# Kernel optimization log

Hardware: AMD Instinct MI355X
Metric: run time of the kernel (lower is better)

Reference implementation:

```python
import jax, jax.numpy as jnp
import numpy as np
import math

EPS = 1e-5

def _ln(x, g, b):
    m = jnp.mean(x, axis=-1, keepdims=True)
    v = jnp.var(x, axis=-1, keepdims=True)
    return (x - m) * jax.lax.rsqrt(v + EPS) * g + b

def _rn_layer(x, W, g, b, A, Bb, Rw):
    # x: (B,S,in) -> (B,S,out). W: (out,in), A: (out,basis), Bb: (basis,out)
    S = x.shape[1]
    basis_dim = Bb.shape[0]
    n = _ln(x @ W.T, g, b)                      # (B,S,out)
    j = jnp.arange(S) % basis_dim               # (S,)
    Bv = Bb[j]                                  # (S,out)
    scal = jnp.einsum('bsd,sd->bs', n, Bv)      # (B,S)
    Av = A[:, j].T                              # (S,out)
    nf = scal[..., None] * Av                   # (B,S,out)
    res = x if Rw is None else x @ Rw.T
    return nf + res

def _ts_layer(x, M, g, b, P, Rw):
    # x: (B,S,in) -> (B,S,out). M: (out,in), P: (out,out,G)
    S = x.shape[1]
    D, _, G = P.shape
    t = _ln(x @ M.T, g, b)                      # (B,S,out)
    k = jnp.arange(S, dtype=jnp.float32)
    periods = (jnp.arange(D, dtype=jnp.float32)[:, None, None] * (D * G)
               + jnp.arange(D, dtype=jnp.float32)[None, :, None] * G
               + jnp.arange(G, dtype=jnp.float32)[None, None, :] + 2.0)  # (D,D,G)
    phi = jnp.cos(2.0 * math.pi * k[:, None, None, None] / periods)       # (S,D,D,G)
    # Nk[b,s,i] = sum_{j,g} P[i,j,g] * t[b,s,j] * phi[s,i,j,g]
    Wp = jnp.einsum('ijg,sijg->sij', P, phi)    # (S,D,D)
    Nk = jnp.einsum('sij,bsj->bsi', Wp, t)      # (B,S,D)
    return Nk + x @ Rw.T

def setup_inputs() -> dict:
    key = jax.random.key(0)
    ks = jax.random.split(key, 16)
    B, S = 2, 2048
    d0, d1, d2 = 512, 64, 512        # input_dim, ts out, final out
    bas1, G, bas3 = 64, 8, 64
    u = lambda k, sh, a: jax.random.uniform(k, sh, jnp.float32, -a, a)
    inp = {
        'x':  jax.random.normal(ks[0], (B, S, d0), jnp.float32),
        # Layer 1: RN 512->512 (in==out -> no residual proj)
        'W1': u(ks[1], (d0, d0), 0.1),
        'g1': jnp.ones((d0,), jnp.float32),
        'b1': jnp.zeros((d0,), jnp.float32),
        'A1': u(ks[2], (d0, bas1), 0.1),
        'B1': u(ks[3], (bas1, d0), 0.1),
        # Layer 2: TS 512->64
        'M2': u(ks[4], (d1, d0), 0.5),
        'g2': jnp.ones((d1,), jnp.float32),
        'b2': jnp.zeros((d1,), jnp.float32),
        'P2': u(ks[5], (d1, d1, G), 0.1),
        'R2': u(ks[6], (d1, d0), 0.1),
        # Layer 3: RN 64->512
        'W3': u(ks[7], (d2, d1), 0.1),
        'g3': jnp.ones((d2,), jnp.float32),
        'b3': jnp.zeros((d2,), jnp.float32),
        'A3': u(ks[8], (d2, bas3), 0.1),
        'B3': u(ks[9], (bas3, d2), 0.1),
        'R3': u(ks[10], (d2, d1), 0.1),
    }
    return inp

def reference(x, W1, g1, b1, A1, B1, M2, g2, b2, P2, R2, W3, g3, b3, A3, B3, R3):
    h = _rn_layer(x, W1, g1, b1, A1, B1, None)   # (B,S,512), identity residual
    h = _ts_layer(h, M2, g2, b2, P2, R2)         # (B,S,64)
    h = _rn_layer(h, W3, g3, b3, A3, B3, R3)     # (B,S,512)
    return h
```

## Files before the change

### kernel.cpp

```cpp
#include <hip/hip_runtime.h>
#include <math.h>

#define SEQ  2048
#define ROWS 4096
#define D0   512
#define D1   64

typedef short bf8 __attribute__((ext_vector_type(8)));
typedef float f4  __attribute__((ext_vector_type(4)));

__device__ __forceinline__ unsigned short f2bf(float f) {
    unsigned u = __float_as_uint(f);
    return (unsigned short)((u + 0x7fffu + ((u >> 16) & 1u)) >> 16);
}
__device__ __forceinline__ float bf2f(unsigned short u) {
    return __uint_as_float((unsigned)u << 16);
}
__device__ __forceinline__ void hilo(float f, unsigned short& h, unsigned short& l) {
    h = f2bf(f);
    float fh = bf2f(h);
    l = f2bf(f - fh);
}
__device__ __forceinline__ void cv4h(unsigned short* dh, int idx, float4 v) {
    ushort4 hv;
    hv.x = f2bf(v.x); hv.y = f2bf(v.y); hv.z = f2bf(v.z); hv.w = f2bf(v.w);
    *(ushort4*)(dh + idx) = hv;
}

__device__ __forceinline__ void async16(const void* g, void* l) {
    __builtin_amdgcn_global_load_lds(
        (const __attribute__((address_space(1))) unsigned int*)g,
        (__attribute__((address_space(3))) unsigned int*)l, 16, 0, 0);
}

__global__ __launch_bounds__(256) void convk(
        const float* __restrict__ x,  const float* __restrict__ W1,
        const float* __restrict__ M2, const float* __restrict__ R2,
        const float* __restrict__ W3, const float* __restrict__ R3,
        const float* __restrict__ A1, const float* __restrict__ A3,
        unsigned short* __restrict__ xh,
        unsigned short* __restrict__ W1h,
        unsigned short* __restrict__ C2h,
        unsigned short* __restrict__ C3h,
        float* __restrict__ A1T, float* __restrict__ A3T) {
    int c = blockIdx.x, tid = threadIdx.x;
    if (c < 1216) {
        const float* src; unsigned short* dh; int off;
        if      (c < 1024) { src = x;  dh = xh;          off = c; }
        else if (c < 1152) { src = W1; dh = W1h;         off = c - 1024; }
        else if (c < 1168) { src = M2; dh = C2h;         off = c - 1152; }
        else if (c < 1184) { src = R2; dh = C2h + 32768; off = c - 1168; }
        else if (c < 1200) { src = W3; dh = C3h;         off = c - 1184; }
        else               { src = R3; dh = C3h + 32768; off = c - 1200; }
        int base = off * 2048 + tid * 4;
        cv4h(dh, base,        *(const float4*)(src + base));
        cv4h(dh, base + 1024, *(const float4*)(src + base + 1024));
    } else {
        int gid = (c - 1216) * 256 + tid;
        int i = gid >> 6, j = gid & 63;
        A1T[j * 512 + i] = A1[gid];
        A3T[j * 512 + i] = A3[gid];
    }
}

template<bool ALO, int OM>
__global__ __launch_bounds__(256, 4) void gemm128t(
        const unsigned short* __restrict__ Ah, const unsigned short* __restrict__ Al,
        const unsigned short* __restrict__ Wh,
        float* __restrict__ Cf, unsigned short* __restrict__ Cb,
        int M, int N, int K, int Ks) {
    __shared__ __align__(16) unsigned short aH[8192];
    __shared__ __align__(16) unsigned short aL[ALO ? 8192 : 16];
    __shared__ __align__(16) unsigned short wH[4096];
    const int tid = threadIdx.x;
    const int wv  = tid >> 6;
    const int ln  = tid & 63;
    const int lm  = ln & 15;
    const int lq  = ln >> 4;
    const int bm  = blockIdx.y * 128;
    const int bn  = blockIdx.x * 64;
    const int k0  = blockIdx.z * Ks;

    f4 acc[2][4] = {};

    for (int kt = 0; kt < Ks; kt += 64) {
        const int kg = k0 + kt;
        __syncthreads();
#pragma unroll
        for (int i = 0; i < 4; ++i) {
            int slot = i * 256 + wv * 64 + ln;
            int row  = slot >> 3;
            int ch   = (slot & 7) ^ (row & 7);
            size_t go = (size_t)(bm + row) * K + kg + ch * 8;
            async16(Ah + go, aH + slot * 8);
            if constexpr (ALO) async16(Al + go, aL + slot * 8);
        }
#pragma unroll
        for (int i = 0; i < 2; ++i) {
            int slot = i * 256 + wv * 64 + ln;
            int row  = slot >> 3;
            int ch   = (slot & 7) ^ (row & 7);
            size_t go = (size_t)(bn + row) * K + kg + ch * 8;
            async16(Wh + go, wH + slot * 8);
        }
        __syncthreads();

#pragma unroll
        for (int kk = 0; kk < 2; ++kk) {
            const int ck = kk * 4 + lq;
            bf8 a_h[2], a_l[2], b_h[4];
#pragma unroll
            for (int t = 0; t < 2; ++t) {
                int r = wv * 32 + t * 16 + lm;
                a_h[t] = *(const bf8*)(aH + r * 64 + ((ck ^ (r & 7)) * 8));
                if constexpr (ALO)
                    a_l[t] = *(const bf8*)(aL + r * 64 + ((ck ^ (r & 7)) * 8));
            }
#pragma unroll
            for (int u = 0; u < 4; ++u) {
                int rb = u * 16 + lm;
                b_h[u] = *(const bf8*)(wH + rb * 64 + ((ck ^ (rb & 7)) * 8));
            }
#pragma unroll
            for (int t = 0; t < 2; ++t)
#pragma unroll
                for (int u = 0; u < 4; ++u) {
                    acc[t][u] = __builtin_amdgcn_mfma_f32_16x16x32_bf16(a_h[t], b_h[u], acc[t][u], 0, 0, 0);
                    if constexpr (ALO)
                        acc[t][u] = __builtin_amdgcn_mfma_f32_16x16x32_bf16(a_l[t], b_h[u], acc[t][u], 0, 0, 0);
                }
        }
    }

#pragma unroll
    for (int t = 0; t < 2; ++t)
#pragma unroll
        for (int u = 0; u < 4; ++u) {
            int row = bm + wv * 32 + t * 16 + lq * 4;
            int col = bn + u * 16 + lm;
#pragma unroll
            for (int r = 0; r < 4; ++r) {
                float v = acc[t][u][r];
                if constexpr (OM == 0) {
                    Cf[(size_t)blockIdx.z * M * N + (size_t)(row + r) * N + col] = v;
                } else if constexpr (OM == 1) {
                    Cb[(size_t)blockIdx.z * M * N + (size_t)(row + r) * N + col] = f2bf(v);
                } else {
                    if (col < 512) Cb[(size_t)(row + r) * 512 + col] = f2bf(v);
                    else           Cf[(size_t)(row + r) * 512 + col - 512] = v;
                }
            }
        }
}

__global__ __launch_bounds__(256) void lnrn(
        const unsigned short* __restrict__ Yb0,
        const unsigned short* __restrict__ Yb1,
        const float* __restrict__ RES,
        const float* __restrict__ g, const float* __restrict__ be,
        const float* __restrict__ Bb, const float* __restrict__ AaT,
        float* __restrict__ outf,
        unsigned short* __restrict__ outh, unsigned short* __restrict__ outl) {
    const int row = blockIdx.x * 4 + (threadIdx.x >> 6);
    const int l = threadIdx.x & 63;
    const int c = l * 8;
    ushort4 ua = *(const ushort4*)(Yb0 + (size_t)row * D0 + c);
    ushort4 ub = *(const ushort4*)(Yb0 + (size_t)row * D0 + c + 4);
    float4 y0, y1;
    y0.x = bf2f(ua.x); y0.y = bf2f(ua.y); y0.z = bf2f(ua.z); y0.w = bf2f(ua.w);
    y1.x = bf2f(ub.x); y1.y = bf2f(ub.y); y1.z = bf2f(ub.z); y1.w = bf2f(ub.w);
    if (Yb1) {
        ushort4 va = *(const ushort4*)(Yb1 + (size_t)row * D0 + c);
        ushort4 vb = *(const ushort4*)(Yb1 + (size_t)row * D0 + c + 4);
        y0.x += bf2f(va.x); y0.y += bf2f(va.y); y0.z += bf2f(va.z); y0.w += bf2f(va.w);
        y1.x += bf2f(vb.x); y1.y += bf2f(vb.y); y1.z += bf2f(vb.z); y1.w += bf2f(vb.w);
    }
    float sum = y0.x + y0.y + y0.z + y0.w + y1.x + y1.y + y1.z + y1.w;
    float ssq = y0.x*y0.x + y0.y*y0.y + y0.z*y0.z + y0.w*y0.w
              + y1.x*y1.x + y1.y*y1.y + y1.z*y1.z + y1.w*y1.w;
#pragma unroll
    for (int m = 1; m < 64; m <<= 1) {
        sum += __shfl_xor(sum, m, 64);
        ssq += __shfl_xor(ssq, m, 64);
    }
    float mean = sum * (1.0f / 512.0f);
    float var  = ssq * (1.0f / 512.0f) - mean * mean;
    float rstd = rsqrtf(var + 1e-5f);
    float4 g0 = *(const float4*)(g + c),  g1v = *(const float4*)(g + c + 4);
    float4 e0 = *(const float4*)(be + c), e1  = *(const float4*)(be + c + 4);
    float4 n0, n1;
    n0.x = (y0.x - mean) * rstd * g0.x  + e0.x;
    n0.y = (y0.y - mean) * rstd * g0.y  + e0.y;
    n0.z = (y0.z - mean) * rstd * g0.z  + e0.z;
    n0.w = (y0.w - mean) * rstd * g0.w  + e0.w;
    n1.x = (y1.x - mean) * rstd * g1v.x + e1.x;
    n1.y = (y1.y - mean) * rstd * g1v.y + e1.y;
    n1.z = (y1.z - mean) * rstd * g1v.z + e1.z;
    n1.w = (y1.w - mean) * rstd * g1v.w + e1.w;
    const int jm = row & 63;
    const float* bb = Bb + jm * D0 + c;
    float4 b0 = *(const float4*)bb, b1v = *(const float4*)(bb + 4);
    float p = n0.x*b0.x + n0.y*b0.y + n0.z*b0.z + n0.w*b0.w
            + n1.x*b1v.x + n1.y*b1v.y + n1.z*b1v.z + n1.w*b1v.w;
#pragma unroll
    for (int m = 1; m < 64; m <<= 1) p += __shfl_xor(p, m, 64);
    const float* av = AaT + jm * D0 + c;
    float4 a0 = *(const float4*)av, a1 = *(const float4*)(av + 4);
    const float* rs = RES + (size_t)row * D0 + c;
    float4 r0 = *(const float4*)rs, r1 = *(const float4*)(rs + 4);
    float4 v0, v1;
    v0.x = p*a0.x + r0.x; v0.y = p*a0.y + r0.y; v0.z = p*a0.z + r0.z; v0.w = p*a0.w + r0.w;
    v1.x = p*a1.x + r1.x; v1.y = p*a1.y + r1.y; v1.z = p*a1.z + r1.z; v1.w = p*a1.w + r1.w;
    if (outf) {
        *(float4*)(outf + (size_t)row * D0 + c)     = v0;
        *(float4*)(outf + (size_t)row * D0 + c + 4) = v1;
    } else {
        ushort4 h0, l0, h1, l1;
        hilo(v0.x, h0.x, l0.x); hilo(v0.y, h0.y, l0.y);
        hilo(v0.z, h0.z, l0.z); hilo(v0.w, h0.w, l0.w);
        hilo(v1.x, h1.x, l1.x); hilo(v1.y, h1.y, l1.y);
        hilo(v1.z, h1.z, l1.z); hilo(v1.w, h1.w, l1.w);
        *(ushort4*)(outh + (size_t)row * D0 + c)     = h0;
        *(ushort4*)(outl + (size_t)row * D0 + c)     = l0;
        *(ushort4*)(outh + (size_t)row * D0 + c + 4) = h1;
        *(ushort4*)(outl + (size_t)row * D0 + c + 4) = l1;
    }
}

#define C2S 524288
__global__ __launch_bounds__(256) void lnt(
        const float* __restrict__ C2, const float* __restrict__ g2,
        const float* __restrict__ b2,
        float* __restrict__ t, float* __restrict__ rsum) {
    const int r = blockIdx.x * 4 + (threadIdx.x >> 6);
    const int j = threadIdx.x & 63;
    size_t base = (size_t)r * 128 + j;
    float v = 0.f, rv = 0.f;
#pragma unroll
    for (int z = 0; z < 4; ++z) {
        v  += C2[(size_t)z * C2S + base];
        rv += C2[(size_t)z * C2S + base + 64];
    }
    float sum = v, ssq = v * v;
#pragma unroll
    for (int m = 1; m < 64; m <<= 1) {
        sum += __shfl_xor(sum, m, 64);
        ssq += __shfl_xor(ssq, m, 64);
    }
    float mean = sum * (1.0f / 64.0f);
    float var  = ssq * (1.0f / 64.0f) - mean * mean;
    float rstd = rsqrtf(var + 1e-5f);
    t[r * 64 + j]    = (v - mean) * rstd * g2[j] + b2[j];
    rsum[r * 64 + j] = rv;
}

__global__ __launch_bounds__(256) void tsk2(
        const float* __restrict__ t, const float* __restrict__ rsum,
        const float* __restrict__ P,
        unsigned short* __restrict__ Hh, unsigned short* __restrict__ Hl) {
    const int bid = blockIdx.x;
    const int i   = bid >> 3;
    const int sg  = bid & 7;
    const int w   = threadIdx.x >> 6;
    const int ln  = threadIdx.x & 63;
    const int s0  = sg * 256 + w * 64;
    const int idx = i * 64 + ln;
    const float* pp = P + idx * 8;
    const float sf0 = (float)s0;

    float k2c[8], ca[8], cb[8];
#pragma unroll
    for (int g = 0; g < 8; ++g) {
        float pf   = (float)(idx * 8 + g + 2);
        float invp = __builtin_amdgcn_rcpf(pf);
        k2c[g] = 2.0f * __builtin_amdgcn_cosf(invp);
        float q0 = floorf(sf0 * invp);
        float r0 = fmaf(-q0, pf, sf0);
        float f0 = r0 * invp; f0 -= floorf(f0);
        float c0 = __builtin_amdgcn_cosf(f0);
        float sf1 = sf0 + 1.0f;
        float q1 = floorf(sf1 * invp);
        float r1 = fmaf(-q1, pf, sf1);
        float f1 = r1 * invp; f1 -= floorf(f1);
        float c1 = __builtin_amdgcn_cosf(f1);
        float Pv = pp[g];
        ca[g] = Pv * c0;
        cb[g] = Pv * c1;
    }

    const int tb = s0 * 64 + ln;
    float t0c = t[tb], t1c = t[131072 + tb];
    float res0 = 0.f, res1 = 0.f;

    for (int st = 0; st < 64; st += 2) {
        float t0n  = t[tb + (st + 1) * 64];
        float t1n  = t[131072 + tb + (st + 1) * 64];
        float ws = ((ca[0] + ca[1]) + (ca[2] + ca[3]))
                 + ((ca[4] + ca[5]) + (ca[6] + ca[7]));
#pragma unroll
        for (int g = 0; g < 8; ++g) ca[g] = fmaf(k2c[g], cb[g], -ca[g]);
        float v0 = ws * t0c, v1 = ws * t1c;
#pragma unroll
        for (int m = 1; m < 64; m <<= 1) {
            v0 += __shfl_xor(v0, m, 64);
            v1 += __shfl_xor(v1, m, 64);
        }
        res0 = (ln == st) ? v0 : res0;
        res1 = (ln == st) ? v1 : res1;
        float t0n2 = t[tb + (st + 2) * 64];
        float t1n2 = t[131072 + tb + (st + 2) * 64];
        float ws2 = ((cb[0] + cb[1]) + (cb[2] + cb[3]))
                  + ((cb[4] + cb[5]) + (cb[6] + cb[7]));
#pragma unroll
        for (int g = 0; g < 8; ++g) cb[g] = fmaf(k2c[g], ca[g], -cb[g]);
        float v0b = ws2 * t0n, v1b = ws2 * t1n;
#pragma unroll
        for (int m = 1; m < 64; m <<= 1) {
            v0b += __shfl_xor(v0b, m, 64);
            v1b += __shfl_xor(v1b, m, 64);
        }
        res0 = (ln == st + 1) ? v0b : res0;
        res1 = (ln == st + 1) ? v1b : res1;
        t0c = t0n2; t1c = t1n2;
    }

    const int s = s0 + ln;
    {
        float v = res0 + rsum[(size_t)s * 64 + i];
        unsigned short h, l; hilo(v, h, l);
        Hh[(size_t)s * 64 + i] = h; Hl[(size_t)s * 64 + i] = l;
        float v1e = res1 + rsum[(size_t)(SEQ + s) * 64 + i];
        hilo(v1e, h, l);
        Hh[(size_t)(SEQ + s) * 64 + i] = h; Hl[(size_t)(SEQ + s) * 64 + i] = l;
    }
}

extern "C" void kernel_launch(void* const* d_in, const int* in_sizes, int n_in,
                              void* d_out, int out_size, void* d_ws, size_t ws_size,
                              hipStream_t stream) {
    const float* x  = (const float*)d_in[0];
    const float* W1 = (const float*)d_in[1];
    const float* g1 = (const float*)d_in[2];
    const float* b1 = (const float*)d_in[3];
    const float* A1 = (const float*)d_in[4];
    const float* B1 = (const float*)d_in[5];
    const float* M2 = (const float*)d_in[6];
    const float* g2 = (const float*)d_in[7];
    const float* b2 = (const float*)d_in[8];
    const float* P2 = (const float*)d_in[9];
    const float* R2 = (const float*)d_in[10];
    const float* W3 = (const float*)d_in[11];
    const float* g3 = (const float*)d_in[12];
    const float* b3 = (const float*)d_in[13];
    const float* A3 = (const float*)d_in[14];
    const float* B3 = (const float*)d_in[15];
    const float* R3 = (const float*)d_in[16];

    float* ws = (float*)d_ws;
    float* C2   = ws;
    float* C3r  = ws + 2097152;
    float* t    = ws + 4194304;
    float* rsum = ws + 4456448;
    float* A1T  = ws + 4718592;
    float* A3T  = ws + 4751360;
    unsigned short* us = (unsigned short*)(ws + 4784128);
    unsigned short* xh   = us;
    unsigned short* h1h  = us + 2097152;
    unsigned short* h1l  = us + 4194304;
    unsigned short* W1h  = us + 6291456;
    unsigned short* Wc2h = us + 6553600;
    unsigned short* Wc3h = us + 6619136;
    unsigned short* h2h  = us + 6684672;
    unsigned short* h2l  = us + 6946816;
    unsigned short* C1b  = us + 7208960;
    unsigned short* C3n  = us + 11403264;

    dim3 blk(256);

    convk<<<1344, blk, 0, stream>>>(x, W1, M2, R2, W3, R3, A1, A3,
                                    xh, W1h, Wc2h, Wc3h, A1T, A3T);

    gemm128t<false, 1><<<dim3(8, 32, 2), blk, 0, stream>>>(
        xh, xh, W1h, nullptr, C1b, ROWS, 512, 512, 256);
    lnrn<<<1024, blk, 0, stream>>>(C1b, C1b + (size_t)ROWS * 512, x,
                                   g1, b1, B1, A1T, nullptr, h1h, h1l);

    gemm128t<true, 0><<<dim3(2, 32, 4), blk, 0, stream>>>(
        h1h, h1l, Wc2h, C2, nullptr, ROWS, 128, 512, 128);
    lnt<<<1024, blk, 0, stream>>>(C2, g2, b2, t, rsum);
    tsk2<<<512, blk, 0, stream>>>(t, rsum, P2, h2h, h2l);

    gemm128t<true, 2><<<dim3(16, 32, 1), blk, 0, stream>>>(
        h2h, h2l, Wc3h, C3r, C3n, ROWS, 1024, 64, 64);
    lnrn<<<1024, blk, 0, stream>>>(C3n, nullptr, C3r, g3, b3, B3, A3T,
                                   (float*)d_out, nullptr, nullptr);
}
```

Measured before the change: 152.1 us.

## Fuse all stages into one cooperative persistent megakernel with grid syncs

Replaces the eight separate kernel launches with a single cooperative kernel of 256 blocks of 512 threads, in which each block acts as two virtual 256-thread workers and the stages are separated by grid.sync(). The goal is to remove per-launch overhead and inter-kernel gaps. The cost is that the GEMM tiles are remapped onto a fixed 256-block grid, which changes occupancy: each block uses a larger LDS footprint and 512 threads. Some stages leave blocks idle, for example the second GEMM uses only 128 blocks. If the cooperative launch fails, the code falls back to the old multi-kernel path.

```diff
diff --git a/kernel.cpp b/kernel.cpp
--- a/kernel.cpp
+++ b/kernel.cpp
@@ -1,10 +1,14 @@
 #include <hip/hip_runtime.h>
+#include <hip/hip_cooperative_groups.h>
 #include <math.h>
+
+namespace cg = cooperative_groups;
 
 #define SEQ  2048
 #define ROWS 4096
 #define D0   512
 #define D1   64
+#define C2S  524288
 
 typedef short bf8 __attribute__((ext_vector_type(8)));
 typedef float f4  __attribute__((ext_vector_type(4)));
@@ -31,6 +35,383 @@
     __builtin_amdgcn_global_load_lds(
         (const __attribute__((address_space(1))) unsigned int*)g,
         (__attribute__((address_space(3))) unsigned int*)l, 16, 0, 0);
+}
+
+struct KArgs {
+    const float *x, *W1, *g1, *b1, *A1, *B1;
+    const float *M2, *g2, *b2, *P2, *R2;
+    const float *W3, *g3, *b3, *A3, *B3, *R3;
+    float* out;
+    float* ws;
+};
+
+__device__ __forceinline__ void conv_v(int c, int tid, const KArgs& a,
+        unsigned short* xh, unsigned short* W1h,
+        unsigned short* C2h, unsigned short* C3h,
+        float* A1T, float* A3T) {
+    if (c < 1216) {
+        const float* src; unsigned short* dh; int off;
+        if      (c < 1024) { src = a.x;  dh = xh;          off = c; }
+        else if (c < 1152) { src = a.W1; dh = W1h;         off = c - 1024; }
+        else if (c < 1168) { src = a.M2; dh = C2h;         off = c - 1152; }
+        else if (c < 1184) { src = a.R2; dh = C2h + 32768; off = c - 1168; }
+        else if (c < 1200) { src = a.W3; dh = C3h;         off = c - 1184; }
+        else               { src = a.R3; dh = C3h + 32768; off = c - 1200; }
+        int base = off * 2048 + tid * 4;
+        cv4h(dh, base,        *(const float4*)(src + base));
+        cv4h(dh, base + 1024, *(const float4*)(src + base + 1024));
+    } else {
+        int gid = (c - 1216) * 256 + tid;
+        int i = gid >> 6, j = gid & 63;
+        A1T[j * 512 + i] = a.A1[gid];
+        A3T[j * 512 + i] = a.A3[gid];
+    }
+}
+
+template<bool ALO, int OM>
+__device__ __forceinline__ void gemm512(
+        const unsigned short* __restrict__ Ah, const unsigned short* __restrict__ Al,
+        const unsigned short* __restrict__ Wh,
+        float* __restrict__ Cf, unsigned short* __restrict__ Cb,
+        int N, int K, int Ks, int bm, int bn, int k0,
+        unsigned short* aH, unsigned short* aL, unsigned short* wHh) {
+    const int t   = threadIdx.x;
+    const int tid = t & 255;
+    const int ln  = t & 63;
+    const int wv  = (t >> 6) & 3;
+    const int lm  = ln & 15;
+    const int lq  = ln >> 4;
+
+    f4 acc[2][4] = {};
+
+    for (int kt = 0; kt < Ks; kt += 64) {
+        const int kg = k0 + kt;
+        __syncthreads();
+#pragma unroll
+        for (int i = 0; i < 2; ++i) {
+            int slot = i * 512 + t;
+            int row  = slot >> 3;
+            int ch   = (slot & 7) ^ (row & 7);
+            size_t go = (size_t)(bm + row) * K + kg + ch * 8;
+            async16(Ah + go, aH + slot * 8);
+            if constexpr (ALO) async16(Al + go, aL + slot * 8);
+        }
+#pragma unroll
+        for (int i = 0; i < 2; ++i) {
+            int slot = i * 256 + tid;
+            int row  = slot >> 3;
+            int ch   = (slot & 7) ^ (row & 7);
+            size_t go = (size_t)(bn + row) * K + kg + ch * 8;
+            async16(Wh + go, wHh + slot * 8);
+        }
+        __syncthreads();
+
+#pragma unroll
+        for (int kk = 0; kk < 2; ++kk) {
+            const int ck = kk * 4 + lq;
+            bf8 a_h[2], a_l[2], b_h[4];
+#pragma unroll
+            for (int t2 = 0; t2 < 2; ++t2) {
+                int r = wv * 32 + t2 * 16 + lm;
+                a_h[t2] = *(const bf8*)(aH + r * 64 + ((ck ^ (r & 7)) * 8));
+                if constexpr (ALO)
+                    a_l[t2] = *(const bf8*)(aL + r * 64 + ((ck ^ (r & 7)) * 8));
+            }
+#pragma unroll
+            for (int u = 0; u < 4; ++u) {
+                int rb = u * 16 + lm;
+                b_h[u] = *(const bf8*)(wHh + rb * 64 + ((ck ^ (rb & 7)) * 8));
+            }
+#pragma unroll
+            for (int t2 = 0; t2 < 2; ++t2)
+#pragma unroll
+                for (int u = 0; u < 4; ++u) {
+                    acc[t2][u] = __builtin_amdgcn_mfma_f32_16x16x32_bf16(a_h[t2], b_h[u], acc[t2][u], 0, 0, 0);
+                    if constexpr (ALO)
+                        acc[t2][u] = __builtin_amdgcn_mfma_f32_16x16x32_bf16(a_l[t2], b_h[u], acc[t2][u], 0, 0, 0);
+                }
+        }
+    }
+
+#pragma unroll
+    for (int t2 = 0; t2 < 2; ++t2)
+#pragma unroll
+        for (int u = 0; u < 4; ++u) {
+            int row = bm + wv * 32 + t2 * 16 + lq * 4;
+            int col = bn + u * 16 + lm;
+#pragma unroll
+            for (int r = 0; r < 4; ++r) {
+                float v = acc[t2][u][r];
+                if constexpr (OM == 0) {
+                    Cf[(size_t)(row + r) * N + col] = v;
+                } else if constexpr (OM == 1) {
+                    Cb[(size_t)(row + r) * N + col] = f2bf(v);
+                } else {
+                    if (col < 512) Cb[(size_t)(row + r) * 512 + col] = f2bf(v);
+                    else           Cf[(size_t)(row + r) * 512 + col - 512] = v;
+                }
+            }
+        }
+}
+
+__device__ __forceinline__ void lnrn_v(int vb,
+        const unsigned short* __restrict__ Yb0,
+        const unsigned short* __restrict__ Yb1,
+        const float* __restrict__ RES,
+        const float* __restrict__ g, const float* __restrict__ be,
+        const float* __restrict__ Bb, const float* __restrict__ AaT,
+        float* __restrict__ outf,
+        unsigned short* __restrict__ outh, unsigned short* __restrict__ outl) {
+    const int row = vb * 4 + ((threadIdx.x >> 6) & 3);
+    const int l = threadIdx.x & 63;
+    const int c = l * 8;
+    ushort4 ua = *(const ushort4*)(Yb0 + (size_t)row * D0 + c);
+    ushort4 ub = *(const ushort4*)(Yb0 + (size_t)row * D0 + c + 4);
+    float4 y0, y1;
+    y0.x = bf2f(ua.x); y0.y = bf2f(ua.y); y0.z = bf2f(ua.z); y0.w = bf2f(ua.w);
+    y1.x = bf2f(ub.x); y1.y = bf2f(ub.y); y1.z = bf2f(ub.z); y1.w = bf2f(ub.w);
+    if (Yb1) {
+        ushort4 va = *(const ushort4*)(Yb1 + (size_t)row * D0 + c);
+        ushort4 vb2 = *(const ushort4*)(Yb1 + (size_t)row * D0 + c + 4);
+        y0.x += bf2f(va.x); y0.y += bf2f(va.y); y0.z += bf2f(va.z); y0.w += bf2f(va.w);
+        y1.x += bf2f(vb2.x); y1.y += bf2f(vb2.y); y1.z += bf2f(vb2.z); y1.w += bf2f(vb2.w);
+    }
+    float sum = y0.x + y0.y + y0.z + y0.w + y1.x + y1.y + y1.z + y1.w;
+    float ssq = y0.x*y0.x + y0.y*y0.y + y0.z*y0.z + y0.w*y0.w
+              + y1.x*y1.x + y1.y*y1.y + y1.z*y1.z + y1.w*y1.w;
+#pragma unroll
+    for (int m = 1; m < 64; m <<= 1) {
+        sum += __shfl_xor(sum, m, 64);
+        ssq += __shfl_xor(ssq, m, 64);
+    }
+    float mean = sum * (1.0f / 512.0f);
+    float var  = ssq * (1.0f / 512.0f) - mean * mean;
+    float rstd = rsqrtf(var + 1e-5f);
+    float4 g0 = *(const float4*)(g + c),  g1v = *(const float4*)(g + c + 4);
+    float4 e0 = *(const float4*)(be + c), e1  = *(const float4*)(be + c + 4);
+    float4 n0, n1;
+    n0.x = (y0.x - mean) * rstd * g0.x  + e0.x;
+    n0.y = (y0.y - mean) * rstd * g0.y  + e0.y;
+    n0.z = (y0.z - mean) * rstd * g0.z  + e0.z;
+    n0.w = (y0.w - mean) * rstd * g0.w  + e0.w;
+    n1.x = (y1.x - mean) * rstd * g1v.x + e1.x;
+    n1.y = (y1.y - mean) * rstd * g1v.y + e1.y;
+    n1.z = (y1.z - mean) * rstd * g1v.z + e1.z;
+    n1.w = (y1.w - mean) * rstd * g1v.w + e1.w;
+    const int jm = row & 63;
+    const float* bb = Bb + jm * D0 + c;
+    float4 b0 = *(const float4*)bb, b1v = *(const float4*)(bb + 4);
+    float p = n0.x*b0.x + n0.y*b0.y + n0.z*b0.z + n0.w*b0.w
+            + n1.x*b1v.x + n1.y*b1v.y + n1.z*b1v.z + n1.w*b1v.w;
+#pragma unroll
+    for (int m = 1; m < 64; m <<= 1) p += __shfl_xor(p, m, 64);
+    const float* av = AaT + jm * D0 + c;
+    float4 a0 = *(const float4*)av, a1 = *(const float4*)(av + 4);
+    const float* rs = RES + (size_t)row * D0 + c;
+    float4 r0 = *(const float4*)rs, r1 = *(const float4*)(rs + 4);
+    float4 v0, v1;
+    v0.x = p*a0.x + r0.x; v0.y = p*a0.y + r0.y; v0.z = p*a0.z + r0.z; v0.w = p*a0.w + r0.w;
+    v1.x = p*a1.x + r1.x; v1.y = p*a1.y + r1.y; v1.z = p*a1.z + r1.z; v1.w = p*a1.w + r1.w;
+    if (outf) {
+        *(float4*)(outf + (size_t)row * D0 + c)     = v0;
+        *(float4*)(outf + (size_t)row * D0 + c + 4) = v1;
+    } else {
+        ushort4 h0, l0, h1, l1;
+        hilo(v0.x, h0.x, l0.x); hilo(v0.y, h0.y, l0.y);
+        hilo(v0.z, h0.z, l0.z); hilo(v0.w, h0.w, l0.w);
+        hilo(v1.x, h1.x, l1.x); hilo(v1.y, h1.y, l1.y);
+        hilo(v1.z, h1.z, l1.z); hilo(v1.w, h1.w, l1.w);
+        *(ushort4*)(outh + (size_t)row * D0 + c)     = h0;
+        *(ushort4*)(outl + (size_t)row * D0 + c)     = l0;
+        *(ushort4*)(outh + (size_t)row * D0 + c + 4) = h1;
+        *(ushort4*)(outl + (size_t)row * D0 + c + 4) = l1;
+    }
+}
+
+__device__ __forceinline__ void lnt_v(int vb,
+        const float* __restrict__ C2, const float* __restrict__ g2,
+        const float* __restrict__ b2,
+        float* __restrict__ tv, float* __restrict__ rsum) {
+    const int r = vb * 4 + ((threadIdx.x >> 6) & 3);
+    const int j = threadIdx.x & 63;
+    size_t base = (size_t)r * 128 + j;
+    float v = 0.f, rv = 0.f;
+#pragma unroll
+    for (int z = 0; z < 4; ++z) {
+        v  += C2[(size_t)z * C2S + base];
+        rv += C2[(size_t)z * C2S + base + 64];
+    }
+    float sum = v, ssq = v * v;
+#pragma unroll
+    for (int m = 1; m < 64; m <<= 1) {
+        sum += __shfl_xor(sum, m, 64);
+        ssq += __shfl_xor(ssq, m, 64);
+    }
+    float mean = sum * (1.0f / 64.0f);
+    float var  = ssq * (1.0f / 64.0f) - mean * mean;
+    float rstd = rsqrtf(var + 1e-5f);
+    tv[r * 64 + j]   = (v - mean) * rstd * g2[j] + b2[j];
+    rsum[r * 64 + j] = rv;
+}
+
+__device__ __forceinline__ void tsk2_v(int vb,
+        const float* __restrict__ tv, const float* __restrict__ rsum,
+        const float* __restrict__ P,
+        unsigned short* __restrict__ Hh, unsigned short* __restrict__ Hl) {
+    const int i   = vb >> 3;
+    const int sg  = vb & 7;
+    const int w   = (threadIdx.x >> 6) & 3;
+    const int ln  = threadIdx.x & 63;
+    const int s0  = sg * 256 + w * 64;
+    const int idx = i * 64 + ln;
+    const float* pp = P + idx * 8;
+    const float sf0 = (float)s0;
+
+    float k2c[8], ca[8], cb[8];
+#pragma unroll
+    for (int g = 0; g < 8; ++g) {
+        float pf   = (float)(idx * 8 + g + 2);
+        float invp = __builtin_amdgcn_rcpf(pf);
+        k2c[g] = 2.0f * __builtin_amdgcn_cosf(invp);
+        float q0 = floorf(sf0 * invp);
+        float r0 = fmaf(-q0, pf, sf0);
+        float f0 = r0 * invp; f0 -= floorf(f0);
+        float c0 = __builtin_amdgcn_cosf(f0);
+        float sf1 = sf0 + 1.0f;
+        float q1 = floorf(sf1 * invp);
+        float r1 = fmaf(-q1, pf, sf1);
+        float f1 = r1 * invp; f1 -= floorf(f1);
+        float c1 = __builtin_amdgcn_cosf(f1);
+        float Pv = pp[g];
+        ca[g] = Pv * c0;
+        cb[g] = Pv * c1;
+    }
+
+    const int tb = s0 * 64 + ln;
+    float t0c = tv[tb], t1c = tv[131072 + tb];
+    float res0 = 0.f, res1 = 0.f;
+
+    for (int st = 0; st < 64; st += 2) {
+        float t0n  = tv[tb + (st + 1) * 64];
+        float t1n  = tv[131072 + tb + (st + 1) * 64];
+        float ws = ((ca[0] + ca[1]) + (ca[2] + ca[3]))
+                 + ((ca[4] + ca[5]) + (ca[6] + ca[7]));
+#pragma unroll
+        for (int g = 0; g < 8; ++g) ca[g] = fmaf(k2c[g], cb[g], -ca[g]);
+        float v0 = ws * t0c, v1 = ws * t1c;
+#pragma unroll
+        for (int m = 1; m < 64; m <<= 1) {
+            v0 += __shfl_xor(v0, m, 64);
+            v1 += __shfl_xor(v1, m, 64);
+        }
+        res0 = (ln == st) ? v0 : res0;
+        res1 = (ln == st) ? v1 : res1;
+        float t0n2 = tv[tb + (st + 2) * 64];
+        float t1n2 = tv[131072 + tb + (st + 2) * 64];
+        float ws2 = ((cb[0] + cb[1]) + (cb[2] + cb[3]))
+                  + ((cb[4] + cb[5]) + (cb[6] + cb[7]));
+#pragma unroll
+        for (int g = 0; g < 8; ++g) cb[g] = fmaf(k2c[g], ca[g], -cb[g]);
+        float v0b = ws2 * t0n, v1b = ws2 * t1n;
+#pragma unroll
+        for (int m = 1; m < 64; m <<= 1) {
+            v0b += __shfl_xor(v0b, m, 64);
+            v1b += __shfl_xor(v1b, m, 64);
+        }
+        res0 = (ln == st + 1) ? v0b : res0;
+        res1 = (ln == st + 1) ? v1b : res1;
+        t0c = t0n2; t1c = t1n2;
+    }
+
+    const int s = s0 + ln;
+    {
+        float v = res0 + rsum[(size_t)s * 64 + i];
+        unsigned short h, l; hilo(v, h, l);
+        Hh[(size_t)s * 64 + i] = h; Hl[(size_t)s * 64 + i] = l;
+        float v1e = res1 + rsum[(size_t)(SEQ + s) * 64 + i];
+        hilo(v1e, h, l);
+        Hh[(size_t)(SEQ + s) * 64 + i] = h; Hl[(size_t)(SEQ + s) * 64 + i] = l;
+    }
+}
+
+__global__ __launch_bounds__(512) void megak(KArgs a) {
+    cg::grid_group grid = cg::this_grid();
+    const int t    = threadIdx.x;
+    const int half = t >> 8;
+    const int tid  = t & 255;
+    const int bid  = blockIdx.x;
+    const int wid  = bid * 2 + half;
+
+    __shared__ __align__(16) unsigned short aH[8192];
+    __shared__ __align__(16) unsigned short aL[8192];
+    __shared__ __align__(16) unsigned short wH[2][4096];
+
+    float* ws   = a.ws;
+    float* C2   = ws;
+    float* C3r  = ws + 2097152;
+    float* tbuf = ws + 4194304;
+    float* rsum = ws + 4456448;
+    float* A1T  = ws + 4718592;
+    float* A3T  = ws + 4751360;
+    unsigned short* us = (unsigned short*)(ws + 4784128);
+    unsigned short* xh   = us;
+    unsigned short* h1h  = us + 2097152;
+    unsigned short* h1l  = us + 4194304;
+    unsigned short* W1h  = us + 6291456;
+    unsigned short* Wc2h = us + 6553600;
+    unsigned short* Wc3h = us + 6619136;
+    unsigned short* h2h  = us + 6684672;
+    unsigned short* h2l  = us + 6946816;
+    unsigned short* C1b  = us + 7208960;
+    unsigned short* C3n  = us + 11403264;
+
+    for (int c = wid; c < 1344; c += 512)
+        conv_v(c, tid, a, xh, W1h, Wc2h, Wc3h, A1T, A3T);
+    grid.sync();
+
+    {
+        int bn = (bid & 3) * 128 + half * 64;
+        int bm = ((bid >> 2) & 31) * 128;
+        int bz = bid >> 7;
+        gemm512<false, 1>(xh, xh, W1h, nullptr,
+                          C1b + (size_t)bz * ROWS * 512,
+                          512, 512, 256, bm, bn, bz * 256, aH, aL, wH[half]);
+    }
+    grid.sync();
+
+    for (int vb = wid; vb < 1024; vb += 512)
+        lnrn_v(vb, C1b, C1b + (size_t)ROWS * 512, a.x, a.g1, a.b1, a.B1, A1T,
+               nullptr, h1h, h1l);
+    grid.sync();
+
+    if (bid < 128) {
+        int bn = half * 64;
+        int bm = (bid & 31) * 128;
+        int bz = bid >> 5;
+        gemm512<true, 0>(h1h, h1l, Wc2h,
+                         C2 + (size_t)bz * C2S, nullptr,
+                         128, 512, 128, bm, bn, bz * 128, aH, aL, wH[half]);
+    }
+    grid.sync();
+
+    for (int vb = wid; vb < 1024; vb += 512)
+        lnt_v(vb, C2, a.g2, a.b2, tbuf, rsum);
+    grid.sync();
+
+    tsk2_v(wid, tbuf, rsum, a.P2, h2h, h2l);
+    grid.sync();
+
+    {
+        int bn = (bid & 7) * 128 + half * 64;
+        int bm = ((bid >> 3) & 31) * 128;
+        gemm512<true, 2>(h2h, h2l, Wc3h, C3r, C3n,
+                         1024, 64, 64, bm, bn, 0, aH, aL, wH[half]);
+    }
+    grid.sync();
+
+    for (int vb = wid; vb < 1024; vb += 512)
+        lnrn_v(vb, C3n, nullptr, C3r, a.g3, a.b3, a.B3, A3T,
+               a.out, nullptr, nullptr);
 }
 
 __global__ __launch_bounds__(256) void convk(
@@ -71,7 +452,7 @@
         int M, int N, int K, int Ks) {
     __shared__ __align__(16) unsigned short aH[8192];
     __shared__ __align__(16) unsigned short aL[ALO ? 8192 : 16];
-    __shared__ __align__(16) unsigned short wH[4096];
+    __shared__ __align__(16) unsigned short wHs[4096];
     const int tid = threadIdx.x;
     const int wv  = tid >> 6;
     const int ln  = tid & 63;
@@ -101,7 +482,7 @@
             int row  = slot >> 3;
             int ch   = (slot & 7) ^ (row & 7);
             size_t go = (size_t)(bn + row) * K + kg + ch * 8;
-            async16(Wh + go, wH + slot * 8);
+            async16(Wh + go, wHs + slot * 8);
         }
         __syncthreads();
 
@@ -119,7 +500,7 @@
 #pragma unroll
             for (int u = 0; u < 4; ++u) {
                 int rb = u * 16 + lm;
-                b_h[u] = *(const bf8*)(wH + rb * 64 + ((ck ^ (rb & 7)) * 8));
+                b_h[u] = *(const bf8*)(wHs + rb * 64 + ((ck ^ (rb & 7)) * 8));
             }
 #pragma unroll
             for (int t = 0; t < 2; ++t)
@@ -161,200 +542,53 @@
         const float* __restrict__ Bb, const float* __restrict__ AaT,
         float* __restrict__ outf,
         unsigned short* __restrict__ outh, unsigned short* __restrict__ outl) {
-    const int row = blockIdx.x * 4 + (threadIdx.x >> 6);
-    const int l = threadIdx.x & 63;
-    const int c = l * 8;
-    ushort4 ua = *(const ushort4*)(Yb0 + (size_t)row * D0 + c);
-    ushort4 ub = *(const ushort4*)(Yb0 + (size_t)row * D0 + c + 4);
-    float4 y0, y1;
-    y0.x = bf2f(ua.x); y0.y = bf2f(ua.y); y0.z = bf2f(ua.z); y0.w = bf2f(ua.w);
-    y1.x = bf2f(ub.x); y1.y = bf2f(ub.y); y1.z = bf2f(ub.z); y1.w = bf2f(ub.w);
-    if (Yb1) {
-        ushort4 va = *(const ushort4*)(Yb1 + (size_t)row * D0 + c);
-        ushort4 vb = *(const ushort4*)(Yb1 + (size_t)row * D0 + c + 4);
-        y0.x += bf2f(va.x); y0.y += bf2f(va.y); y0.z += bf2f(va.z); y0.w += bf2f(va.w);
-        y1.x += bf2f(vb.x); y1.y += bf2f(vb.y); y1.z += bf2f(vb.z); y1.w += bf2f(vb.w);
-    }
-    float sum = y0.x + y0.y + y0.z + y0.w + y1.x + y1.y + y1.z + y1.w;
-    float ssq = y0.x*y0.x + y0.y*y0.y + y0.z*y0.z + y0.w*y0.w
-              + y1.x*y1.x + y1.y*y1.y + y1.z*y1.z + y1.w*y1.w;
-#pragma unroll
-    for (int m = 1; m < 64; m <<= 1) {
-        sum += __shfl_xor(sum, m, 64);
-        ssq += __shfl_xor(ssq, m, 64);
-    }
-    float mean = sum * (1.0f / 512.0f);
-    float var  = ssq * (1.0f / 512.0f) - mean * mean;
-    float rstd = rsqrtf(var + 1e-5f);
-    float4 g0 = *(const float4*)(g + c),  g1v = *(const float4*)(g + c + 4);
-    float4 e0 = *(const float4*)(be + c), e1  = *(const float4*)(be + c + 4);
-    float4 n0, n1;
-    n0.x = (y0.x - mean) * rstd * g0.x  + e0.x;
-    n0.y = (y0.y - mean) * rstd * g0.y  + e0.y;
-    n0.z = (y0.z - mean) * rstd * g0.z  + e0.z;
-    n0.w = (y0.w - mean) * rstd * g0.w  + e0.w;
-    n1.x = (y1.x - mean) * rstd * g1v.x + e1.x;
-    n1.y = (y1.y - mean) * rstd * g1v.y + e1.y;
-    n1.z = (y1.z - mean) * rstd * g1v.z + e1.z;
-    n1.w = (y1.w - mean) * rstd * g1v.w + e1.w;
-    const int jm = row & 63;
-    const float* bb = Bb + jm * D0 + c;
-    float4 b0 = *(const float4*)bb, b1v = *(const float4*)(bb + 4);
-    float p = n0.x*b0.x + n0.y*b0.y + n0.z*b0.z + n0.w*b0.w
-            + n1.x*b1v.x + n1.y*b1v.y + n1.z*b1v.z + n1.w*b1v.w;
-#pragma unroll
-    for (int m = 1; m < 64; m <<= 1) p += __shfl_xor(p, m, 64);
-    const float* av = AaT + jm * D0 + c;
-    float4 a0 = *(const float4*)av, a1 = *(const float4*)(av + 4);
-    const float* rs = RES + (size_t)row * D0 + c;
-    float4 r0 = *(const float4*)rs, r1 = *(const float4*)(rs + 4);
-    float4 v0, v1;
-    v0.x = p*a0.x + r0.x; v0.y = p*a0.y + r0.y; v0.z = p*a0.z + r0.z; v0.w = p*a0.w + r0.w;
-    v1.x = p*a1.x + r1.x; v1.y = p*a1.y + r1.y; v1.z = p*a1.z + r1.z; v1.w = p*a1.w + r1.w;
-    if (outf) {
-        *(float4*)(outf + (size_t)row * D0 + c)     = v0;
-        *(float4*)(outf + (size_t)row * D0 + c + 4) = v1;
-    } else {
-        ushort4 h0, l0, h1, l1;
-        hilo(v0.x, h0.x, l0.x); hilo(v0.y, h0.y, l0.y);
-        hilo(v0.z, h0.z, l0.z); hilo(v0.w, h0.w, l0.w);
-        hilo(v1.x, h1.x, l1.x); hilo(v1.y, h1.y, l1.y);
-        hilo(v1.z, h1.z, l1.z); hilo(v1.w, h1.w, l1.w);
-        *(ushort4*)(outh + (size_t)row * D0 + c)     = h0;
-        *(ushort4*)(outl + (size_t)row * D0 + c)     = l0;
-        *(ushort4*)(outh + (size_t)row * D0 + c + 4) = h1;
-        *(ushort4*)(outl + (size_t)row * D0 + c + 4) = l1;
-    }
-}
-
-#define C2S 524288
+    lnrn_v(blockIdx.x, Yb0, Yb1, RES, g, be, Bb, AaT, outf, outh, outl);
+}
+
 __global__ __launch_bounds__(256) void lnt(
         const float* __restrict__ C2, const float* __restrict__ g2,
         const float* __restrict__ b2,
         float* __restrict__ t, float* __restrict__ rsum) {
-    const int r = blockIdx.x * 4 + (threadIdx.x >> 6);
-    const int j = threadIdx.x & 63;
-    size_t base = (size_t)r * 128 + j;
-    float v = 0.f, rv = 0.f;
-#pragma unroll
-    for (int z = 0; z < 4; ++z) {
-        v  += C2[(size_t)z * C2S + base];
-        rv += C2[(size_t)z * C2S + base + 64];
-    }
-    float sum = v, ssq = v * v;
-#pragma unroll
-    for (int m = 1; m < 64; m <<= 1) {
-        sum += __shfl_xor(sum, m, 64);
-        ssq += __shfl_xor(ssq, m, 64);
-    }
-    float mean = sum * (1.0f / 64.0f);
-    float var  = ssq * (1.0f / 64.0f) - mean * mean;
-    float rstd = rsqrtf(var + 1e-5f);
-    t[r * 64 + j]    = (v - mean) * rstd * g2[j] + b2[j];
-    rsum[r * 64 + j] = rv;
+    lnt_v(blockIdx.x, C2, g2, b2, t, rsum);
 }
 
 __global__ __launch_bounds__(256) void tsk2(
         const float* __restrict__ t, const float* __restrict__ rsum,
         const float* __restrict__ P,
         unsigned short* __restrict__ Hh, unsigned short* __restrict__ Hl) {
-    const int bid = blockIdx.x;
-    const int i   = bid >> 3;
-    const int sg  = bid & 7;
-    const int w   = threadIdx.x >> 6;
-    const int ln  = threadIdx.x & 63;
-    const int s0  = sg * 256 + w * 64;
-    const int idx = i * 64 + ln;
-    const float* pp = P + idx * 8;
-    const float sf0 = (float)s0;
-
-    float k2c[8], ca[8], cb[8];
-#pragma unroll
-    for (int g = 0; g < 8; ++g) {
-        float pf   = (float)(idx * 8 + g + 2);
-        float invp = __builtin_amdgcn_rcpf(pf);
-        k2c[g] = 2.0f * __builtin_amdgcn_cosf(invp);
-        float q0 = floorf(sf0 * invp);
-        float r0 = fmaf(-q0, pf, sf0);
-        float f0 = r0 * invp; f0 -= floorf(f0);
-        float c0 = __builtin_amdgcn_cosf(f0);
-        float sf1 = sf0 + 1.0f;
-        float q1 = floorf(sf1 * invp);
-        float r1 = fmaf(-q1, pf, sf1);
-        float f1 = r1 * invp; f1 -= floorf(f1);
-        float c1 = __builtin_amdgcn_cosf(f1);
-        float Pv = pp[g];
-        ca[g] = Pv * c0;
-        cb[g] = Pv * c1;
-    }
-
-    const int tb = s0 * 64 + ln;
-    float t0c = t[tb], t1c = t[131072 + tb];
-    float res0 = 0.f, res1 = 0.f;
-
-    for (int st = 0; st < 64; st += 2) {
-        float t0n  = t[tb + (st + 1) * 64];
-        float t1n  = t[131072 + tb + (st + 1) * 64];
-        float ws = ((ca[0] + ca[1]) + (ca[2] + ca[3]))
-                 + ((ca[4] + ca[5]) + (ca[6] + ca[7]));
-#pragma unroll
-        for (int g = 0; g < 8; ++g) ca[g] = fmaf(k2c[g], cb[g], -ca[g]);
-        float v0 = ws * t0c, v1 = ws * t1c;
-#pragma unroll
-        for (int m = 1; m < 64; m <<= 1) {
-            v0 += __shfl_xor(v0, m, 64);
-            v1 += __shfl_xor(v1, m, 64);
-        }
-        res0 = (ln == st) ? v0 : res0;
-        res1 = (ln == st) ? v1 : res1;
-        float t0n2 = t[tb + (st + 2) * 64];
-        float t1n2 = t[131072 + tb + (st + 2) * 64];
-        float ws2 = ((cb[0] + cb[1]) + (cb[2] + cb[3]))
-                  + ((cb[4] + cb[5]) + (cb[6] + cb[7]));
-#pragma unroll
-        for (int g = 0; g < 8; ++g) cb[g] = fmaf(k2c[g], ca[g], -cb[g]);
-        float v0b = ws2 * t0n, v1b = ws2 * t1n;
-#pragma unroll
-        for (int m = 1; m < 64; m <<= 1) {
-            v0b += __shfl_xor(v0b, m, 64);
-            v1b += __shfl_xor(v1b, m, 64);
-        }
-        res0 = (ln == st + 1) ? v0b : res0;
-        res1 = (ln == st + 1) ? v1b : res1;
-        t0c = t0n2; t1c = t1n2;
-    }
-
-    const int s = s0 + ln;
-    {
-        float v = res0 + rsum[(size_t)s * 64 + i];
-        unsigned short h, l; hilo(v, h, l);
-        Hh[(size_t)s * 64 + i] = h; Hl[(size_t)s * 64 + i] = l;
-        float v1e = res1 + rsum[(size_t)(SEQ + s) * 64 + i];
-        hilo(v1e, h, l);
-        Hh[(size_t)(SEQ + s) * 64 + i] = h; Hl[(size_t)(SEQ + s) * 64 + i] = l;
-    }
+    tsk2_v(blockIdx.x, t, rsum, P, Hh, Hl);
 }
 
 extern "C" void kernel_launch(void* const* d_in, const int* in_sizes, int n_in,
                               void* d_out, int out_size, void* d_ws, size_t ws_size,
                               hipStream_t stream) {
-    const float* x  = (const float*)d_in[0];
-    const float* W1 = (const float*)d_in[1];
-    const float* g1 = (const float*)d_in[2];
-    const float* b1 = (const float*)d_in[3];
-    const float* A1 = (const float*)d_in[4];
-    const float* B1 = (const float*)d_in[5];
-    const float* M2 = (const float*)d_in[6];
-    const float* g2 = (const float*)d_in[7];
-    const float* b2 = (const float*)d_in[8];
-    const float* P2 = (const float*)d_in[9];
-    const float* R2 = (const float*)d_in[10];
-    const float* W3 = (const float*)d_in[11];
-    const float* g3 = (const float*)d_in[12];
-    const float* b3 = (const float*)d_in[13];
-    const float* A3 = (const float*)d_in[14];
-    const float* B3 = (const float*)d_in[15];
-    const float* R3 = (const float*)d_in[16];
+    (void)in_sizes; (void)n_in; (void)out_size; (void)ws_size;
+    KArgs a;
+    a.x  = (const float*)d_in[0];
+    a.W1 = (const float*)d_in[1];
+    a.g1 = (const float*)d_in[2];
+    a.b1 = (const float*)d_in[3];
+    a.A1 = (const float*)d_in[4];
+    a.B1 = (const float*)d_in[5];
+    a.M2 = (const float*)d_in[6];
+    a.g2 = (const float*)d_in[7];
+    a.b2 = (const float*)d_in[8];
+    a.P2 = (const float*)d_in[9];
+    a.R2 = (const float*)d_in[10];
+    a.W3 = (const float*)d_in[11];
+    a.g3 = (const float*)d_in[12];
+    a.b3 = (const float*)d_in[13];
+    a.A3 = (const float*)d_in[14];
+    a.B3 = (const float*)d_in[15];
+    a.R3 = (const float*)d_in[16];
+    a.out = (float*)d_out;
+    a.ws  = (float*)d_ws;
+
+    void* kargs[] = { (void*)&a };
+    hipError_t e = hipLaunchCooperativeKernel((const void*)megak,
+                                              dim3(256), dim3(512),
+                                              kargs, 0, stream);
+    if (e == hipSuccess) return;
 
     float* ws = (float*)d_ws;
     float* C2   = ws;
@@ -376,22 +610,18 @@
     unsigned short* C3n  = us + 11403264;
 
     dim3 blk(256);
-
-    convk<<<1344, blk, 0, stream>>>(x, W1, M2, R2, W3, R3, A1, A3,
+    convk<<<1344, blk, 0, stream>>>(a.x, a.W1, a.M2, a.R2, a.W3, a.R3, a.A1, a.A3,
                                     xh, W1h, Wc2h, Wc3h, A1T, A3T);
-
     gemm128t<false, 1><<<dim3(8, 32, 2), blk, 0, stream>>>(
         xh, xh, W1h, nullptr, C1b, ROWS, 512, 512, 256);
-    lnrn<<<1024, blk, 0, stream>>>(C1b, C1b + (size_t)ROWS * 512, x,
-                                   g1, b1, B1, A1T, nullptr, h1h, h1l);
-
+    lnrn<<<1024, blk, 0, stream>>>(C1b, C1b + (size_t)ROWS * 512, a.x,
+                                   a.g1, a.b1, a.B1, A1T, nullptr, h1h, h1l);
     gemm128t<true, 0><<<dim3(2, 32, 4), blk, 0, stream>>>(
         h1h, h1l, Wc2h, C2, nullptr, ROWS, 128, 512, 128);
-    lnt<<<1024, blk, 0, stream>>>(C2, g2, b2, t, rsum);
-    tsk2<<<512, blk, 0, stream>>>(t, rsum, P2, h2h, h2l);
-
+    lnt<<<1024, blk, 0, stream>>>(C2, a.g2, a.b2, t, rsum);
+    tsk2<<<512, blk, 0, stream>>>(t, rsum, a.P2, h2h, h2l);
     gemm128t<true, 2><<<dim3(16, 32, 1), blk, 0, stream>>>(
         h2h, h2l, Wc3h, C3r, C3n, ROWS, 1024, 64, 64);
-    lnrn<<<1024, blk, 0, stream>>>(C3n, nullptr, C3r, g3, b3, B3, A3T,
+    lnrn<<<1024, blk, 0, stream>>>(C3n, nullptr, C3r, a.g3, a.b3, a.B3, A3T,
                                    (float*)d_out, nullptr, nullptr);
 }
```

After: 398.6 us. 2.62x slower.
